# Kernel optimization log

Hardware: AMD Instinct MI355X
Metric: run time of the kernel (lower is better)

The kernel has to match this reference:

```python
import jax, jax.numpy as jnp
import numpy as np

N = 50000      # num nodes
E = 400000     # directed edges (avg out-degree 8)
DIN = 128
DOUT = 128
ALPHA = 0.5    # args.alphaDir (buffer, requires_grad=False)
BETA = 0.5     # args.betaDir
GAMA = 0.5     # args.gamaDir


def _dedupe(rows, cols, vals, n):
    key = rows.astype(np.int64) * n + cols.astype(np.int64)
    uk, inv = np.unique(key, return_inverse=True)
    v = np.bincount(inv, weights=vals, minlength=uk.shape[0])
    return (uk // n).astype(np.int32), (uk % n).astype(np.int32), v.astype(np.float32)


def _dir_norm(r, c, v, n):
    # directed_norm: D_out^{-1/2} A D_in^{-1/2}, inf -> 0
    in_deg = np.bincount(c, weights=v, minlength=n)
    out_deg = np.bincount(r, weights=v, minlength=n)
    in_is = np.zeros(n); m = in_deg > 0; in_is[m] = in_deg[m] ** -0.5
    out_is = np.zeros(n); m = out_deg > 0; out_is[m] = out_deg[m] ** -0.5
    return r, c, (out_is[r] * v * in_is[c]).astype(np.float32)


def _spgemm(rA, cA, vA, rB, cB, vB, n):
    # sparse @ sparse in COO, vectorized numpy
    order = np.argsort(rB, kind='stable')
    rBs, cBs, vBs = rB[order], cB[order], vB[order]
    degB = np.bincount(rBs, minlength=n)
    indptr = np.concatenate(([0], np.cumsum(degB)))
    counts = degB[cA]
    total = int(counts.sum())
    rep = np.repeat(np.arange(len(rA)), counts)
    first = np.cumsum(counts) - counts
    pos = np.arange(total) - np.repeat(first, counts) + np.repeat(indptr[cA], counts)
    rows = rA[rep]
    cols = cBs[pos]
    vals = vA[rep].astype(np.float64) * vBs[pos]
    return _dedupe(rows, cols, vals, n)


def setup_inputs() -> dict:
    rng = np.random.default_rng(0)
    r0 = rng.integers(0, N, E).astype(np.int64)
    c0 = rng.integers(0, N, E).astype(np.int64)
    r, c, v = _dedupe(r0, c0, np.ones(E, np.float32), N)
    a = _dir_norm(r, c, v, N)                 # adj_norm
    at = _dir_norm(c, r, v, N)                # adj_t_norm
    rr, cc, vv = _spgemm(a[0], a[1], a[2], at[0], at[1], at[2], N)
    aat = _dir_norm(rr, cc, vv, N)            # directed_norm(A @ At)
    rr, cc, vv = _spgemm(at[0], at[1], at[2], a[0], a[1], a[2], N)
    ata = _dir_norm(rr, cc, vv, N)            # directed_norm(At @ A)
    rr, cc, vv = _spgemm(a[0], a[1], a[2], a[0], a[1], a[2], N)
    aa = _dir_norm(rr, cc, vv, N)             # directed_norm(A @ A)
    rr, cc, vv = _spgemm(at[0], at[1], at[2], at[0], at[1], at[2], N)
    atat = _dir_norm(rr, cc, vv, N)           # directed_norm(At @ At)

    key = jax.random.key(0)
    ks = jax.random.split(key, 7)
    x = jax.random.normal(ks[0], (N, DIN), dtype=jnp.float32)
    s = 1.0 / np.sqrt(DIN)

    def lin(k):
        k1, k2 = jax.random.split(k)
        w = jax.random.uniform(k1, (DIN, DOUT), jnp.float32, -s, s)
        b = jax.random.uniform(k2, (DOUT,), jnp.float32, -s, s)
        return w, b

    w_sd, b_sd = lin(ks[1]); w_ds, b_ds = lin(ks[2])
    w0, b0 = lin(ks[3]); w1, b1 = lin(ks[4])
    w2, b2 = lin(ks[5]); w3, b3 = lin(ks[6])

    out = {'x': x,
           'w_sd': w_sd, 'b_sd': b_sd, 'w_ds': w_ds, 'b_ds': b_ds,
           'w0': w0, 'b0': b0, 'w1': w1, 'b1': b1,
           'w2': w2, 'b2': b2, 'w3': w3, 'b3': b3}
    for name, t in (('a', a), ('at', at), ('aat', aat), ('ata', ata), ('aa', aa), ('atat', atat)):
        out[name + '_rows'] = jnp.asarray(t[0])
        out[name + '_cols'] = jnp.asarray(t[1])
        out[name + '_vals'] = jnp.asarray(t[2])
    return out


def _spmm(rows, cols, vals, x):
    # (A @ x)[i] = sum_e vals[e] * x[cols[e]] scattered to rows[e]
    return jax.ops.segment_sum(vals[:, None] * x[cols], rows, num_segments=x.shape[0])


def reference(x, a_rows, a_cols, a_vals, at_rows, at_cols, at_vals,
              aat_rows, aat_cols, aat_vals, ata_rows, ata_cols, ata_vals,
              aa_rows, aa_cols, aa_vals, atat_rows, atat_cols, atat_vals,
              w_sd, b_sd, w_ds, b_ds, w0, b0, w1, b1, w2, b2, w3, b3):
    out1 = ALPHA * (_spmm(a_rows, a_cols, a_vals, x) @ w_sd + b_sd) \
         + (1.0 - ALPHA) * (_spmm(at_rows, at_cols, at_vals, x) @ w_ds + b_ds)
    out2 = BETA * (_spmm(aat_rows, aat_cols, aat_vals, x) @ w0 + b0) \
         + (1.0 - BETA) * (_spmm(ata_rows, ata_cols, ata_vals, x) @ w1 + b1)
    out3 = GAMA * (_spmm(aa_rows, aa_cols, aa_vals, x) @ w2 + b2) \
         + (1.0 - GAMA) * (_spmm(atat_rows, atat_cols, atat_vals, x) @ w3 + b3)
    return out1 + out2 + out3
```

## Files before the change

kernel.cpp:

```cpp
#include <hip/hip_runtime.h>
#include <hip/hip_bf16.h>

#define FD 128

typedef __attribute__((ext_vector_type(8))) short bf16x8;
typedef __attribute__((ext_vector_type(4))) float f32x4;

__device__ __forceinline__ float bfu2f(unsigned short u) {
  return __uint_as_float(((unsigned int)u) << 16);
}
__device__ __forceinline__ float b2f(__hip_bfloat16 v) { return __bfloat162float(v); }
__device__ __forceinline__ unsigned int pk2(float lo, float hi) {
  return (unsigned int)__bfloat16_as_ushort(__float2bfloat16(lo)) |
         ((unsigned int)__bfloat16_as_ushort(__float2bfloat16(hi)) << 16);
}

__device__ __forceinline__ float ldf(const void* p, int i, int ff) {
  return ff ? ((const float*)p)[i] : b2f(((const __hip_bfloat16*)p)[i]);
}
__device__ __forceinline__ int ldi(const void* p, int i, int fi) {
  return fi ? (int)((const long long*)p)[i] : ((const int*)p)[i];
}

__global__ void detect_k(const void* x, const void* cols, int* flags) {
  __shared__ int cnt[2];
  if (threadIdx.x < 2) cnt[threadIdx.x] = 0;
  __syncthreads();
  const unsigned short* xu = (const unsigned short*)x;
  int big = 0;
  for (int i = threadIdx.x; i < 1024; i += 256) {
    int e = (xu[i] >> 7) & 0xFF;
    if (e >= 0x90) big++;
  }
  if (big) atomicAdd(&cnt[0], big);
  const int* ci = (const int*)cols;
  int zeros = 0;
  for (int i = threadIdx.x; i < 128; i += 256)
    if ((i & 1) && ci[i] == 0) zeros++;
  if (zeros) atomicAdd(&cnt[1], zeros);
  __syncthreads();
  if (threadIdx.x == 0) {
    flags[0] = (cnt[0] > 16) ? 1 : 0;
    flags[1] = (cnt[1] >= 32) ? 1 : 0;
  }
}

__global__ void cvtall_k(const void* __restrict__ rows, const void* __restrict__ cols,
                         const void* __restrict__ vals, int nnz, int n,
                         int* __restrict__ r32, int* __restrict__ c32,
                         float* __restrict__ vf, int* __restrict__ cntT,
                         const int* flags) {
  int ff = flags[0], fi = flags[1];
  int i = blockIdx.x * 256 + threadIdx.x;
  if (i >= nnz) return;
  int r = ldi(rows, i, fi);
  int c = ldi(cols, i, fi);
  if ((unsigned)r >= (unsigned)n) r = 0;
  if ((unsigned)c >= (unsigned)n) c = 0;
  r32[i] = r;
  c32[i] = c;
  vf[i] = ldf(vals, i, ff);
  atomicAdd(&cntT[c], 1);
}

__global__ void scanA_k(const int* __restrict__ cnt, int n, int* bsum) {
  __shared__ int sh[256];
  int t = threadIdx.x;
  int i = blockIdx.x * 256 + t;
  sh[t] = (i < n) ? cnt[i] : 0;
  __syncthreads();
  for (int d = 128; d > 0; d >>= 1) {
    if (t < d) sh[t] += sh[t + d];
    __syncthreads();
  }
  if (t == 0) bsum[blockIdx.x] = sh[0];
}

__global__ void scanB_k(int* bsum, int nb, int* rpTail) {
  __shared__ int sh[256];
  int t = threadIdx.x;
  int v = (t < nb) ? bsum[t] : 0;
  sh[t] = v;
  __syncthreads();
  int val = v;
  for (int d = 1; d < 256; d <<= 1) {
    int add = (t >= d) ? sh[t - d] : 0;
    __syncthreads();
    val += add;
    sh[t] = val;
    __syncthreads();
  }
  if (t < nb) bsum[t] = val - v;
  if (t == 255) *rpTail = val;
}

__global__ void scanC_k(const int* __restrict__ cnt, int n, const int* __restrict__ bsum,
                        int* rp, int* cur) {
  __shared__ int sh[256];
  int t = threadIdx.x;
  int i = blockIdx.x * 256 + t;
  int v = (i < n) ? cnt[i] : 0;
  sh[t] = v;
  __syncthreads();
  int val = v;
  for (int d = 1; d < 256; d <<= 1) {
    int add = (t >= d) ? sh[t - d] : 0;
    __syncthreads();
    val += add;
    sh[t] = val;
    __syncthreads();
  }
  int ex = val - v + bsum[blockIdx.x];
  if (i < n) { rp[i] = ex; cur[i] = ex; }
}

__global__ void bsearch_k(const int* __restrict__ rows, int nnz, int n, int* rpA) {
  int i = blockIdx.x * 256 + threadIdx.x;
  if (i > n) return;
  int lo = 0, hi = nnz;
  while (lo < hi) { int mid = (lo + hi) >> 1; if (rows[mid] < i) lo = mid + 1; else hi = mid; }
  rpA[i] = lo;
}

__global__ void scatter_k(const int* __restrict__ r, const int* __restrict__ c,
                          const float* __restrict__ v, int nnz,
                          int* cur, int* tSrc, float* tVal) {
  int i = blockIdx.x * 256 + threadIdx.x;
  if (i >= nnz) return;
  int p = atomicAdd(&cur[c[i]], 1);
  if ((unsigned)p >= (unsigned)nnz) return;
  tSrc[p] = r[i];
  tVal[p] = v[i];
}

__global__ void nodesum_k(const int* __restrict__ rpA, const float* __restrict__ av,
                          const int* __restrict__ rpT, const float* __restrict__ tv,
                          float* __restrict__ u1, float* __restrict__ v1, int n) {
  int i = blockIdx.x * 256 + threadIdx.x;
  if (i >= n) return;
  float su = 0.f;
  int e0 = rpA[i], e1 = rpA[i + 1];
  for (int j = e0; j < e1; ++j) su += av[j];
  u1[i] = su;
  float sv = 0.f;
  int f0 = rpT[i], f1 = rpT[i + 1];
  for (int j = f0; j < f1; ++j) sv += tv[j];
  v1[i] = sv;
}

__global__ void deg2c_k(const int* __restrict__ rpA, const int* __restrict__ ci,
                        const float* __restrict__ av,
                        const int* __restrict__ rpT, const int* __restrict__ ti,
                        const float* __restrict__ tv,
                        const float* __restrict__ u1, const float* __restrict__ v1,
                        float* __restrict__ s1, float* __restrict__ s2,
                        float* __restrict__ s3, float* __restrict__ s4, int n) {
  int i = blockIdx.x * 256 + threadIdx.x;
  if (i >= n) return;
  float a1 = 0.f, a3 = 0.f;
  int s0 = rpA[i], se = rpA[i + 1];
  for (int j = s0; j < se; ++j) {
    int c = ci[j];
    float v = av[j];
    a1 = fmaf(v, v1[c], a1);
    a3 = fmaf(v, u1[c], a3);
  }
  s1[i] = (a1 > 0.f) ? rsqrtf(a1) : 0.f;
  s3[i] = (a3 > 0.f) ? rsqrtf(a3) : 0.f;
  float a2 = 0.f, a4 = 0.f;
  int t0 = rpT[i], t1 = rpT[i + 1];
  for (int j = t0; j < t1; ++j) {
    int r = ti[j];
    float v = tv[j];
    a2 = fmaf(v, u1[r], a2);
    a4 = fmaf(v, v1[r], a4);
  }
  s2[i] = (a2 > 0.f) ? rsqrtf(a2) : 0.f;
  s4[i] = (a4 > 0.f) ? rsqrtf(a4) : 0.f;
}

__global__ void bias_k(const void* a, const void* b, const void* c, const void* d,
                       const void* e, const void* f, float* bias, const int* flags) {
  int ff = flags[0];
  int i = threadIdx.x;
  bias[i] = 0.5f * (ldf(a, i, ff) + ldf(b, i, ff) + ldf(c, i, ff)
                  + ldf(d, i, ff) + ldf(e, i, ff) + ldf(f, i, ff));
}

__global__ void fill_k(unsigned short* o, int n) {
  int i = blockIdx.x * 256 + threadIdx.x;
  if (i < n) o[i] = 0x3E80;
}

__global__ void cvtx_k(const void* __restrict__ x, __hip_bfloat16* __restrict__ xb,
                       int n, const int* flags) {
  int ff = flags[0];
  int i = (blockIdx.x * 256 + threadIdx.x) * 4;
  if (i + 3 >= n) {
    for (int k = i; k < n; ++k) xb[k] = __float2bfloat16(ldf(x, k, ff));
    return;
  }
  xb[i + 0] = __float2bfloat16(ldf(x, i + 0, ff));
  xb[i + 1] = __float2bfloat16(ldf(x, i + 1, ff));
  xb[i + 2] = __float2bfloat16(ldf(x, i + 2, ff));
  xb[i + 3] = __float2bfloat16(ldf(x, i + 3, ff));
}

struct W6p { const void* w[6]; };
__global__ void wt2_k(W6p ws, __hip_bfloat16* __restrict__ Wt, const int* flags) {
  int ff = flags[0];
  int e = blockIdx.x * 256 + threadIdx.x;
  if (e >= 6 * 16384) return;
  int seg = e >> 14;
  int r = e & 16383;
  int n = r >> 7;
  int innerB = (r & 127) << 1;
  int kb = innerB ^ ((n & 7) << 4);
  int k = kb >> 1;
  Wt[e] = __float2bfloat16(ldf(ws.w[seg], k * 128 + n, ff));
}

struct FHSet {
  const int* rp; const int* ci; const float* cv;
  unsigned int* ot; unsigned int* oa; unsigned int* ob;
  const float* sA; const float* sB;
};

__global__ __launch_bounds__(256) void fh3d_k(
    FHSet h0, FHSet h1, const unsigned int* __restrict__ xb, int n, int half) {
  int blk = blockIdx.x;
  bool hi = blk >= half;
  const int* rp = hi ? h1.rp : h0.rp;
  const int* ci = hi ? h1.ci : h0.ci;
  const float* cv = hi ? h1.cv : h0.cv;
  unsigned int* ot = hi ? h1.ot : h0.ot;
  unsigned int* oa = hi ? h1.oa : h0.oa;
  unsigned int* ob = hi ? h1.ob : h0.ob;
  const float* sA = hi ? h1.sA : h0.sA;
  const float* sB = hi ? h1.sB : h0.sB;
  int bb = hi ? blk - half : blk;

  int wave = threadIdx.x >> 6;
  int lane = threadIdx.x & 63;
  int es = lane >> 4;
  int li = lane & 15;
  int r = bb * 4 + wave;
  if (r >= n) return;
  int s = rp[r], e = rp[r + 1];
  float t[8], a[8], b[8];
#pragma unroll
  for (int k = 0; k < 8; ++k) { t[k] = 0.f; a[k] = 0.f; b[k] = 0.f; }
  for (int j = s + es; j < e; j += 4) {
    int c = ci[j];
    float v = cv[j];
    float va = v * sA[c];
    float vb = v * sB[c];
    uint4 u = *(const uint4*)(xb + (size_t)c * 64 + li * 4);
    unsigned int uu[4] = {u.x, u.y, u.z, u.w};
#pragma unroll
    for (int k = 0; k < 4; ++k) {
      float lo = __uint_as_float(uu[k] << 16);
      float hi2 = __uint_as_float(uu[k] & 0xFFFF0000u);
      t[2 * k]     = fmaf(v, lo, t[2 * k]);
      t[2 * k + 1] = fmaf(v, hi2, t[2 * k + 1]);
      a[2 * k]     = fmaf(va, lo, a[2 * k]);
      a[2 * k + 1] = fmaf(va, hi2, a[2 * k + 1]);
      b[2 * k]     = fmaf(vb, lo, b[2 * k]);
      b[2 * k + 1] = fmaf(vb, hi2, b[2 * k + 1]);
    }
  }
#pragma unroll
  for (int k = 0; k < 8; ++k) {
    t[k] += __shfl_xor(t[k], 16); t[k] += __shfl_xor(t[k], 32);
    a[k] += __shfl_xor(a[k], 16); a[k] += __shfl_xor(a[k], 32);
    b[k] += __shfl_xor(b[k], 16); b[k] += __shfl_xor(b[k], 32);
  }
  if (es == 0) {
    size_t off = (size_t)r * 64 + li * 4;
    uint4 o;
    o.x = pk2(t[0], t[1]); o.y = pk2(t[2], t[3]);
    o.z = pk2(t[4], t[5]); o.w = pk2(t[6], t[7]);
    *(uint4*)(ot + off) = o;
    o.x = pk2(a[0], a[1]); o.y = pk2(a[2], a[3]);
    o.z = pk2(a[4], a[5]); o.w = pk2(a[6], a[7]);
    *(uint4*)(oa + off) = o;
    o.x = pk2(b[0], b[1]); o.y = pk2(b[2], b[3]);
    o.z = pk2(b[4], b[5]); o.w = pk2(b[6], b[7]);
    *(uint4*)(ob + off) = o;
  }
}

struct SHSet {
  const int* rp; const int* ci; const float* cv;
  const unsigned int* ga; const unsigned int* gb;
  unsigned int* ya; unsigned int* yb;
  const float* rsa; const float* rsb;
};

__global__ __launch_bounds__(256) void sh2d_k(SHSet h0, SHSet h1, int n, int half) {
  int blk = blockIdx.x;
  bool hi = blk >= half;
  const int* rp = hi ? h1.rp : h0.rp;
  const int* ci = hi ? h1.ci : h0.ci;
  const float* cv = hi ? h1.cv : h0.cv;
  const unsigned int* ga = hi ? h1.ga : h0.ga;
  const unsigned int* gb = hi ? h1.gb : h0.gb;
  unsigned int* ya = hi ? h1.ya : h0.ya;
  unsigned int* yb = hi ? h1.yb : h0.yb;
  const float* rsa = hi ? h1.rsa : h0.rsa;
  const float* rsb = hi ? h1.rsb : h0.rsb;
  int bb = hi ? blk - half : blk;

  int wave = threadIdx.x >> 6;
  int lane = threadIdx.x & 63;
  int es = lane >> 4;
  int li = lane & 15;
  int r = bb * 4 + wave;
  if (r >= n) return;
  int s = rp[r], e = rp[r + 1];
  float a[8], b[8];
#pragma unroll
  for (int k = 0; k < 8; ++k) { a[k] = 0.f; b[k] = 0.f; }
  for (int j = s + es; j < e; j += 4) {
    int c = ci[j];
    float v = cv[j];
    size_t off = (size_t)c * 64 + li * 4;
    uint4 u = *(const uint4*)(ga + off);
    uint4 w = *(const uint4*)(gb + off);
    unsigned int uu[4] = {u.x, u.y, u.z, u.w};
    unsigned int ww[4] = {w.x, w.y, w.z, w.w};
#pragma unroll
    for (int k = 0; k < 4; ++k) {
      a[2 * k]     = fmaf(v, __uint_as_float(uu[k] << 16), a[2 * k]);
      a[2 * k + 1] = fmaf(v, __uint_as_float(uu[k] & 0xFFFF0000u), a[2 * k + 1]);
      b[2 * k]     = fmaf(v, __uint_as_float(ww[k] << 16), b[2 * k]);
      b[2 * k + 1] = fmaf(v, __uint_as_float(ww[k] & 0xFFFF0000u), b[2 * k + 1]);
    }
  }
#pragma unroll
  for (int k = 0; k < 8; ++k) {
    a[k] += __shfl_xor(a[k], 16); a[k] += __shfl_xor(a[k], 32);
    b[k] += __shfl_xor(b[k], 16); b[k] += __shfl_xor(b[k], 32);
  }
  if (es == 0) {
    float ra = rsa[r], rb = rsb[r];
    size_t off = (size_t)r * 64 + li * 4;
    uint4 o;
    o.x = pk2(a[0] * ra, a[1] * ra); o.y = pk2(a[2] * ra, a[3] * ra);
    o.z = pk2(a[4] * ra, a[5] * ra); o.w = pk2(a[6] * ra, a[7] * ra);
    *(uint4*)(ya + off) = o;
    o.x = pk2(b[0] * rb, b[1] * rb); o.y = pk2(b[2] * rb, b[3] * rb);
    o.z = pk2(b[4] * rb, b[5] * rb); o.w = pk2(b[6] * rb, b[7] * rb);
    *(uint4*)(yb + off) = o;
  }
}

struct Y6 { const unsigned short* y[6]; };

__global__ __launch_bounds__(256) void gemm6m3_k(
    Y6 ys, const unsigned short* __restrict__ Wt2, const float* __restrict__ bias,
    void* __restrict__ outp, int M, const int* flags) {
  int ff = flags[0];
  __shared__ __align__(16) unsigned short Bs[16384];
  const int tid = threadIdx.x;
  const int lane = tid & 63;
  const int wave = tid >> 6;
  const int m = lane & 15;
  const int q = lane >> 4;
  const int r0 = blockIdx.x * 128 + wave * 32;
  const int row0 = r0 + m;
  const int row1 = r0 + 16 + m;
  const bool ok0 = row0 < M;
  const bool ok1 = row1 < M;
  const bf16x8 zero8 = {0, 0, 0, 0, 0, 0, 0, 0};

  f32x4 acc0[8], acc1[8];
#pragma unroll
  for (int nt = 0; nt < 8; ++nt) {
    acc0[nt] = (f32x4){0.f, 0.f, 0.f, 0.f};
    acc1[nt] = (f32x4){0.f, 0.f, 0.f, 0.f};
  }

  bf16x8 Bst[8];
#pragma unroll
  for (int c2 = 0; c2 < 8; ++c2)
    Bst[c2] = *(const bf16x8*)(Wt2 + (size_t)(c2 * 256 + tid) * 8);
  bf16x8 Ap0[4], Ap1[4];
#pragma unroll
  for (int kc = 0; kc < 4; ++kc) {
    Ap0[kc] = ok0 ? *(const bf16x8*)(ys.y[0] + (size_t)row0 * FD + kc * 32 + q * 8) : zero8;
    Ap1[kc] = ok1 ? *(const bf16x8*)(ys.y[0] + (size_t)row1 * FD + kc * 32 + q * 8) : zero8;
  }

  const int swz = (m & 7) << 4;

#pragma unroll
  for (int t = 0; t < 6; ++t) {
    __syncthreads();
#pragma unroll
    for (int c2 = 0; c2 < 8; ++c2)
      *(bf16x8*)((char*)Bs + (size_t)(c2 * 256 + tid) * 16) = Bst[c2];
    bf16x8 A0[4], A1[4];
#pragma unroll
    for (int kc = 0; kc < 4; ++kc) { A0[kc] = Ap0[kc]; A1[kc] = Ap1[kc]; }
    if (t < 5) {
#pragma unroll
      for (int c2 = 0; c2 < 8; ++c2)
        Bst[c2] = *(const bf16x8*)(Wt2 + (size_t)(t + 1) * 16384 +
                                   (size_t)(c2 * 256 + tid) * 8);
#pragma unroll
      for (int kc = 0; kc < 4; ++kc) {
        Ap0[kc] = ok0 ? *(const bf16x8*)(ys.y[t + 1] + (size_t)row0 * FD + kc * 32 + q * 8) : zero8;
        Ap1[kc] = ok1 ? *(const bf16x8*)(ys.y[t + 1] + (size_t)row1 * FD + kc * 32 + q * 8) : zero8;
      }
    }
    __syncthreads();
#pragma unroll
    for (int kc = 0; kc < 4; ++kc) {
      const int koff = (kc * 64 + q * 16) ^ swz;
#pragma unroll
      for (int nt = 0; nt < 8; ++nt) {
        const int nrow = nt * 16 + m;
        bf16x8 bfv = *(const bf16x8*)((const char*)Bs + nrow * 256 + koff);
        acc0[nt] = __builtin_amdgcn_mfma_f32_16x16x32_bf16(A0[kc], bfv, acc0[nt], 0, 0, 0);
        acc1[nt] = __builtin_amdgcn_mfma_f32_16x16x32_bf16(A1[kc], bfv, acc1[nt], 0, 0, 0);
      }
    }
  }

#pragma unroll
  for (int nt = 0; nt < 8; ++nt) {
    int col = nt * 16 + m;
    float bv = bias[col];
#pragma unroll
    for (int rg = 0; rg < 4; ++rg) {
      int g0 = r0 + q * 4 + rg;
      if (g0 < M) {
        float v = 0.5f * acc0[nt][rg] + bv;
        if (ff) ((float*)outp)[(size_t)g0 * FD + col] = v;
        else ((unsigned short*)outp)[(size_t)g0 * FD + col] =
            __bfloat16_as_ushort(__float2bfloat16(v));
      }
      int g1 = r0 + 16 + q * 4 + rg;
      if (g1 < M) {
        float v = 0.5f * acc1[nt][rg] + bv;
        if (ff) ((float*)outp)[(size_t)g1 * FD + col] = v;
        else ((unsigned short*)outp)[(size_t)g1 * FD + col] =
            __bfloat16_as_ushort(__float2bfloat16(v));
      }
    }
  }
}

__global__ __launch_bounds__(128) void spmm_k(
    const int* __restrict__ rp, const void* __restrict__ ci, int cif,
    const void* __restrict__ cv, int cvf,
    const void* __restrict__ x, int xf, __hip_bfloat16* __restrict__ y,
    int n, int nnzMax,
    const float* __restrict__ cscale, const float* __restrict__ rscale,
    const int* flags) {
  int ff = flags[0], fi = flags[1];
  int vf = cvf ? 1 : ff;
  int iw = cif ? fi : 0;
  int xw = xf ? ff : 0;
  const int t = threadIdx.x;
  int r0 = blockIdx.x * 4;
  int rend = min(r0 + 4, n);
  for (int r = r0; r < rend; ++r) {
    int s = rp[r], e = rp[r + 1];
    s = max(0, min(s, nnzMax));
    e = max(s, min(e, nnzMax));
    float acc = 0.f;
    for (int j = s; j < e; ++j) {
      int c = ldi(ci, j, iw);
      if ((unsigned)c >= (unsigned)n) c = 0;
      float v = (vf ? ((const float*)cv)[j] : b2f(((const __hip_bfloat16*)cv)[j]));
      if (cscale) v *= cscale[c];
      float xv = xw ? ((const float*)x)[c * FD + t]
                    : b2f(((const __hip_bfloat16*)x)[c * FD + t]);
      acc = fmaf(v, xv, acc);
    }
    if (rscale) acc *= rscale[r];
    y[r * FD + t] = __float2bfloat16(acc);
  }
}

__global__ __launch_bounds__(256) void gemm_k(
    const __hip_bfloat16* __restrict__ Y, const void* __restrict__ W,
    const float* __restrict__ bias, const void* __restrict__ accin,
    void* __restrict__ outp, int M, const int* flags) {
  int ff = flags[0];
  __shared__ __align__(16) float Wl[32 * 128];
  __shared__ __align__(16) float Yl[64 * 36];
  const int t = threadIdx.x;
  const int row0 = blockIdx.x * 64;
  const int c4 = (t & 31) * 4;
  const int r8 = (t >> 5) * 8;
  const int rs = t >> 3;
  const int q = t & 7;
  float acc[8][4];
#pragma unroll
  for (int m = 0; m < 8; ++m)
#pragma unroll
    for (int j = 0; j < 4; ++j) acc[m][j] = 0.f;
  for (int kc = 0; kc < 4; ++kc) {
    if (ff) {
      const float4* Wg4 = (const float4*)((const float*)W + kc * 32 * 128);
#pragma unroll
      for (int i = 0; i < 4; ++i)
        *(float4*)(Wl + (t + i * 256) * 4) = Wg4[t + i * 256];
    } else {
      const ushort4* Wg4 = (const ushort4*)((const unsigned short*)W + kc * 32 * 128);
#pragma unroll
      for (int i = 0; i < 4; ++i) {
        ushort4 u = Wg4[t + i * 256];
        int base = (t + i * 256) * 4;
        Wl[base + 0] = bfu2f(u.x);
        Wl[base + 1] = bfu2f(u.y);
        Wl[base + 2] = bfu2f(u.z);
        Wl[base + 3] = bfu2f(u.w);
      }
    }
#pragma unroll
    for (int i = 0; i < 2; ++i) {
      int rr = rs + i * 32;
      int grow = row0 + rr;
      ushort4 u = make_ushort4(0, 0, 0, 0);
      if (grow < M)
        u = *(const ushort4*)((const unsigned short*)Y + grow * FD + kc * 32 + q * 4);
      float* yd = Yl + rr * 36 + q * 4;
      yd[0] = bfu2f(u.x); yd[1] = bfu2f(u.y); yd[2] = bfu2f(u.z); yd[3] = bfu2f(u.w);
    }
    __syncthreads();
#pragma unroll
    for (int kk = 0; kk < 32; kk += 4) {
      float4 w0 = *(const float4*)(Wl + (kk + 0) * 128 + c4);
      float4 w1 = *(const float4*)(Wl + (kk + 1) * 128 + c4);
      float4 w2 = *(const float4*)(Wl + (kk + 2) * 128 + c4);
      float4 w3 = *(const float4*)(Wl + (kk + 3) * 128 + c4);
#pragma unroll
      for (int m = 0; m < 8; ++m) {
        float4 yv = *(const float4*)(Yl + (r8 + m) * 36 + kk);
        acc[m][0] = fmaf(yv.x, w0.x, acc[m][0]);
        acc[m][1] = fmaf(yv.x, w0.y, acc[m][1]);
        acc[m][2] = fmaf(yv.x, w0.z, acc[m][2]);
        acc[m][3] = fmaf(yv.x, w0.w, acc[m][3]);
        acc[m][0] = fmaf(yv.y, w1.x, acc[m][0]);
        acc[m][1] = fmaf(yv.y, w1.y, acc[m][1]);
        acc[m][2] = fmaf(yv.y, w1.z, acc[m][2]);
        acc[m][3] = fmaf(yv.y, w1.w, acc[m][3]);
        acc[m][0] = fmaf(yv.z, w2.x, acc[m][0]);
        acc[m][1] = fmaf(yv.z, w2.y, acc[m][1]);
        acc[m][2] = fmaf(yv.z, w2.z, acc[m][2]);
        acc[m][3] = fmaf(yv.z, w2.w, acc[m][3]);
        acc[m][0] = fmaf(yv.w, w3.x, acc[m][0]);
        acc[m][1] = fmaf(yv.w, w3.y, acc[m][1]);
        acc[m][2] = fmaf(yv.w, w3.z, acc[m][2]);
        acc[m][3] = fmaf(yv.w, w3.w, acc[m][3]);
      }
    }
    __syncthreads();
  }
  float4 b4 = make_float4(0.f, 0.f, 0.f, 0.f);
  if (bias) b4 = *(const float4*)(bias + c4);
#pragma unroll
  for (int m = 0; m < 8; ++m) {
    int grow = row0 + r8 + m;
    if (grow >= M) continue;
    float4 rv;
    rv.x = 0.5f * acc[m][0] + b4.x;
    rv.y = 0.5f * acc[m][1] + b4.y;
    rv.z = 0.5f * acc[m][2] + b4.z;
    rv.w = 0.5f * acc[m][3] + b4.w;
    if (accin) {
      if (ff) {
        float4 o = *(const float4*)((const float*)accin + grow * FD + c4);
        rv.x += o.x; rv.y += o.y; rv.z += o.z; rv.w += o.w;
      } else {
        ushort4 o = *(const ushort4*)((const unsigned short*)accin + grow * FD + c4);
        rv.x += bfu2f(o.x); rv.y += bfu2f(o.y); rv.z += bfu2f(o.z); rv.w += bfu2f(o.w);
      }
    }
    if (ff) {
      *(float4*)((float*)outp + grow * FD + c4) = rv;
    } else {
      ushort4 so;
      so.x = __bfloat16_as_ushort(__float2bfloat16(rv.x));
      so.y = __bfloat16_as_ushort(__float2bfloat16(rv.y));
      so.z = __bfloat16_as_ushort(__float2bfloat16(rv.z));
      so.w = __bfloat16_as_ushort(__float2bfloat16(rv.w));
      *(ushort4*)((unsigned short*)outp + grow * FD + c4) = so;
    }
  }
}

extern "C" void kernel_launch(void* const* d_in, const int* in_sizes, int n_in,
                              void* d_out, int out_size, void* d_ws, size_t ws_size,
                              hipStream_t stream) {
  const void* x    = d_in[0];
  const void* w_sd = d_in[1];
  const void* b_sd = d_in[2];
  const void* w_ds = d_in[3];
  const void* b_ds = d_in[4];
  const void* w0   = d_in[5];
  const void* b0   = d_in[6];
  const void* w1   = d_in[7];
  const void* b1   = d_in[8];
  const void* w2   = d_in[9];
  const void* b2   = d_in[10];
  const void* w3   = d_in[11];
  const void* b3   = d_in[12];
  const void* a_rows = d_in[13];
  const void* a_cols = d_in[14];
  const void* a_vals = d_in[15];
  const int nnz = in_sizes[13];
  const int N = in_sizes[0] / FD;

  const size_t BUF = ((size_t)N * FD * 2 + 255) & ~(size_t)255;

  auto misc_need = [&](int nbig) -> size_t {
    size_t need = (size_t)nbig * BUF;
    need += ((size_t)10 * N * 4 + 255) & ~(size_t)255;
    need += 512 + 256 + 1024;
    need += (((size_t)(N + 1) * 4 + 255) & ~(size_t)255) * 2;
    need += (((size_t)N * 4 + 255) & ~(size_t)255) * 2;
    need += (((size_t)nnz * 4 + 255) & ~(size_t)255) * 5;
    need += (6 * 16384 * 2 + 255) & ~(size_t)255;
    return need;
  };
  size_t needA = misc_need(10);
  size_t needB = misc_need(2);

  int pathA = (ws_size >= needA) ? 1 : 0;
  if (!pathA && ws_size < needB) {
    fill_k<<<(out_size + 255) / 256, 256, 0, stream>>>((unsigned short*)d_out, out_size);
    return;
  }

  int nbig = pathA ? 10 : 2;
  char* p = (char*)d_ws;
  char* bufs[10];
  for (int i = 0; i < 10; ++i) bufs[i] = (i < nbig) ? (p + (size_t)i * BUF) : nullptr;
  char* q = p + (size_t)nbig * BUF;
  auto take = [&](size_t bytes) -> char* {
    char* r = q;
    q += (bytes + 255) & ~(size_t)255;
    return r;
  };
  float* degf  = (float*)take((size_t)10 * N * 4);
  float* biasf = (float*)take(512);
  int*   flags = (int*)take(256);
  int*   bsum  = (int*)take(1024);
  int* rpA  = (int*)take((size_t)(N + 1) * 4);
  int* rpT  = (int*)take((size_t)(N + 1) * 4);
  int* curT = (int*)take((size_t)N * 4);
  int* cntT = (int*)take((size_t)N * 4);
  int* tSrc = (int*)take((size_t)nnz * 4);
  float* tValF = (float*)take((size_t)nnz * 4);
  int* aRow32 = (int*)take((size_t)nnz * 4);
  int* aCol32 = (int*)take((size_t)nnz * 4);
  float* aValF = (float*)take((size_t)nnz * 4);
  __hip_bfloat16* Wt = (__hip_bfloat16*)take(6 * 16384 * 2);

  float* u1 = degf;
  float* v1 = degf + N;
  float* s1 = degf + 6 * N;
  float* s2 = degf + 7 * N;
  float* s3 = degf + 8 * N;
  float* s4 = degf + 9 * N;

  int eb = (nnz + 255) / 256;
  int nb = (N + 255) / 256;

  detect_k<<<1, 256, 0, stream>>>(x, a_cols, flags);
  hipMemsetAsync(cntT, 0, (size_t)N * 4, stream);
  cvtall_k<<<eb, 256, 0, stream>>>(a_rows, a_cols, a_vals, nnz, N, aRow32, aCol32, aValF, cntT, flags);
  scanA_k<<<nb, 256, 0, stream>>>(cntT, N, bsum);
  scanB_k<<<1, 256, 0, stream>>>(bsum, nb, rpT + N);
  scanC_k<<<nb, 256, 0, stream>>>(cntT, N, bsum, rpT, curT);
  bsearch_k<<<(N + 256) / 256, 256, 0, stream>>>(aRow32, nnz, N, rpA);
  scatter_k<<<eb, 256, 0, stream>>>(aRow32, aCol32, aValF, nnz, curT, tSrc, tValF);
  nodesum_k<<<nb, 256, 0, stream>>>(rpA, aValF, rpT, tValF, u1, v1, N);
  deg2c_k<<<nb, 256, 0, stream>>>(rpA, aCol32, aValF, rpT, tSrc, tValF, u1, v1,
                                  s1, s2, s3, s4, N);
  bias_k<<<1, FD, 0, stream>>>(b_sd, b_ds, b0, b1, b2, b3, biasf, flags);

  int sg2 = (N + 3) / 4;
  int gg = (N + 63) / 64;
  int gg4 = (N + 127) / 128;

  if (pathA) {
    W6p wargs;
    wargs.w[0] = w_sd; wargs.w[1] = w_ds; wargs.w[2] = w0;
    wargs.w[3] = w1;   wargs.w[4] = w2;   wargs.w[5] = w3;
    wt2_k<<<(6 * 16384 + 255) / 256, 256, 0, stream>>>(wargs, Wt, flags);

    __hip_bfloat16* xb = (__hip_bfloat16*)bufs[0];
    cvtx_k<<<(N * FD / 4 + 255) / 256, 256, 0, stream>>>(x, xb, N * FD, flags);

    unsigned int* xbu = (unsigned int*)bufs[0];
    unsigned int* t2 = (unsigned int*)bufs[1];
    unsigned int* g3 = (unsigned int*)bufs[2];
    unsigned int* g6 = (unsigned int*)bufs[3];
    unsigned int* t1 = (unsigned int*)bufs[4];
    unsigned int* g4 = (unsigned int*)bufs[5];
    unsigned int* g5 = (unsigned int*)bufs[6];
    unsigned int* y3 = (unsigned int*)bufs[7];
    unsigned int* y4 = (unsigned int*)bufs[8];
    unsigned int* y6 = (unsigned int*)bufs[9];
    unsigned int* y5 = (unsigned int*)bufs[0];

    FHSet hT = { rpT, tSrc, tValF, t2, g3, g6, s1, s3 };
    FHSet hA = { rpA, aCol32, aValF, t1, g4, g5, s2, s4 };
    fh3d_k<<<2 * sg2, 256, 0, stream>>>(hT, hA, xbu, N, sg2);

    SHSet sA = { rpA, aCol32, aValF, g3, g5, y3, y5, s1, s3 };
    SHSet sT = { rpT, tSrc, tValF, g4, g6, y4, y6, s2, s4 };
    sh2d_k<<<2 * sg2, 256, 0, stream>>>(sA, sT, N, sg2);

    Y6 yargs;
    yargs.y[0] = (const unsigned short*)t1;
    yargs.y[1] = (const unsigned short*)t2;
    yargs.y[2] = (const unsigned short*)y3;
    yargs.y[3] = (const unsigned short*)y4;
    yargs.y[4] = (const unsigned short*)y5;
    yargs.y[5] = (const unsigned short*)y6;
    gemm6m3_k<<<gg4, 256, 0, stream>>>(yargs, (const unsigned short*)Wt, biasf, d_out, N, flags);
  } else {
    __hip_bfloat16* Yb = (__hip_bfloat16*)bufs[0];
    __hip_bfloat16* gb = (__hip_bfloat16*)bufs[1];
    spmm_k<<<sg2, 128, 0, stream>>>(rpA, a_cols, 1, a_vals, 0, x, 1, Yb, N, nnz, nullptr, nullptr, flags);
    gemm_k<<<gg, 256, 0, stream>>>(Yb, w_sd, biasf, nullptr, d_out, N, flags);
    spmm_k<<<sg2, 128, 0, stream>>>(rpT, tSrc, 0, tValF, 1, x, 1, Yb, N, nnz, nullptr, nullptr, flags);
    gemm_k<<<gg, 256, 0, stream>>>(Yb, w_ds, nullptr, d_out, d_out, N, flags);
    spmm_k<<<sg2, 128, 0, stream>>>(rpT, tSrc, 0, tValF, 1, x, 1, gb, N, nnz, s1, nullptr, flags);
    spmm_k<<<sg2, 128, 0, stream>>>(rpA, a_cols, 1, a_vals, 0, gb, 0, Yb, N, nnz, nullptr, s1, flags);
    gemm_k<<<gg, 256, 0, stream>>>(Yb, w0, nullptr, d_out, d_out, N, flags);
    spmm_k<<<sg2, 128, 0, stream>>>(rpA, a_cols, 1, a_vals, 0, x, 1, gb, N, nnz, s2, nullptr, flags);
    spmm_k<<<sg2, 128, 0, stream>>>(rpT, tSrc, 0, tValF, 1, gb, 0, Yb, N, nnz, nullptr, s2, flags);
    gemm_k<<<gg, 256, 0, stream>>>(Yb, w1, nullptr, d_out, d_out, N, flags);
    spmm_k<<<sg2, 128, 0, stream>>>(rpA, a_cols, 1, a_vals, 0, x, 1, gb, N, nnz, s4, nullptr, flags);
    spmm_k<<<sg2, 128, 0, stream>>>(rpA, a_cols, 1, a_vals, 0, gb, 0, Yb, N, nnz, nullptr, s3, flags);
    gemm_k<<<gg, 256, 0, stream>>>(Yb, w2, nullptr, d_out, d_out, N, flags);
    spmm_k<<<sg2, 128, 0, stream>>>(rpT, tSrc, 0, tValF, 1, x, 1, gb, N, nnz, s3, nullptr, flags);
    spmm_k<<<sg2, 128, 0, stream>>>(rpT, tSrc, 0, tValF, 1, gb, 0, Yb, N, nnz, nullptr, s4, flags);
    gemm_k<<<gg, 256, 0, stream>>>(Yb, w3, nullptr, d_out, d_out, N, flags);
  }
}
```

Baseline: 447.3 us.

## Interleave intermediate pairs, unroll gather loops by two, fuse prep kernels

The two intermediate bf16 tensors read together by the second-hop SpMM are now stored interleaved per row (256 B for one half, then 256 B for the other) in a single buffer. Each gathered neighbour then touches one contiguous 512 B region instead of two separate rows. Both gather loops are unrolled by two so that two neighbour loads are in flight at once. The x conversion, weight transpose and bias sum are merged into a single prep kernel to save launches. The cost is a changed buffer assignment and higher register pressure from the unrolled loops.

Measured after the change: 446.2 us. No clear change (-0.2%).

```diff
diff --git a/kernel.cpp b/kernel.cpp
--- a/kernel.cpp
+++ b/kernel.cpp
@@ -192,32 +192,71 @@
   if (i < n) o[i] = 0x3E80;
 }
 
-__global__ void cvtx_k(const void* __restrict__ x, __hip_bfloat16* __restrict__ xb,
-                       int n, const int* flags) {
+struct W6p { const void* w[6]; };
+struct B6p { const void* b[6]; };
+
+__global__ void prep_k(const void* __restrict__ x, __hip_bfloat16* __restrict__ xb, int nx,
+                       W6p ws, __hip_bfloat16* __restrict__ Wt,
+                       B6p bs, float* __restrict__ bias,
+                       const int* flags, int cvtB) {
   int ff = flags[0];
-  int i = (blockIdx.x * 256 + threadIdx.x) * 4;
-  if (i + 3 >= n) {
-    for (int k = i; k < n; ++k) xb[k] = __float2bfloat16(ldf(x, k, ff));
-    return;
-  }
-  xb[i + 0] = __float2bfloat16(ldf(x, i + 0, ff));
-  xb[i + 1] = __float2bfloat16(ldf(x, i + 1, ff));
-  xb[i + 2] = __float2bfloat16(ldf(x, i + 2, ff));
-  xb[i + 3] = __float2bfloat16(ldf(x, i + 3, ff));
-}
-
-struct W6p { const void* w[6]; };
-__global__ void wt2_k(W6p ws, __hip_bfloat16* __restrict__ Wt, const int* flags) {
-  int ff = flags[0];
-  int e = blockIdx.x * 256 + threadIdx.x;
-  if (e >= 6 * 16384) return;
-  int seg = e >> 14;
-  int r = e & 16383;
-  int n = r >> 7;
-  int innerB = (r & 127) << 1;
-  int kb = innerB ^ ((n & 7) << 4);
-  int k = kb >> 1;
-  Wt[e] = __float2bfloat16(ldf(ws.w[seg], k * 128 + n, ff));
+  int blk = blockIdx.x;
+  if (blk < cvtB) {
+    int i = (blk * 256 + threadIdx.x) * 4;
+    if (i >= nx) return;
+    if (i + 3 >= nx) {
+      for (int k = i; k < nx; ++k) xb[k] = __float2bfloat16(ldf(x, k, ff));
+      return;
+    }
+    xb[i + 0] = __float2bfloat16(ldf(x, i + 0, ff));
+    xb[i + 1] = __float2bfloat16(ldf(x, i + 1, ff));
+    xb[i + 2] = __float2bfloat16(ldf(x, i + 2, ff));
+    xb[i + 3] = __float2bfloat16(ldf(x, i + 3, ff));
+  } else if (blk < cvtB + 384) {
+    int e = (blk - cvtB) * 256 + threadIdx.x;
+    if (e >= 6 * 16384) return;
+    int seg = e >> 14;
+    int r = e & 16383;
+    int n = r >> 7;
+    int innerB = (r & 127) << 1;
+    int kb = innerB ^ ((n & 7) << 4);
+    int k = kb >> 1;
+    Wt[e] = __float2bfloat16(ldf(ws.w[seg], k * 128 + n, ff));
+  } else {
+    int i = threadIdx.x;
+    if (i < FD)
+      bias[i] = 0.5f * (ldf(bs.b[0], i, ff) + ldf(bs.b[1], i, ff) + ldf(bs.b[2], i, ff)
+                      + ldf(bs.b[3], i, ff) + ldf(bs.b[4], i, ff) + ldf(bs.b[5], i, ff));
+  }
+}
+
+__device__ __forceinline__ void fh_fma(const uint4& u, float v, float va, float vb,
+                                       float* t, float* a, float* b) {
+  unsigned int uu[4] = {u.x, u.y, u.z, u.w};
+#pragma unroll
+  for (int k = 0; k < 4; ++k) {
+    float lo = __uint_as_float(uu[k] << 16);
+    float hi = __uint_as_float(uu[k] & 0xFFFF0000u);
+    t[2 * k]     = fmaf(v, lo, t[2 * k]);
+    t[2 * k + 1] = fmaf(v, hi, t[2 * k + 1]);
+    a[2 * k]     = fmaf(va, lo, a[2 * k]);
+    a[2 * k + 1] = fmaf(va, hi, a[2 * k + 1]);
+    b[2 * k]     = fmaf(vb, lo, b[2 * k]);
+    b[2 * k + 1] = fmaf(vb, hi, b[2 * k + 1]);
+  }
+}
+
+__device__ __forceinline__ void sh_fma(const uint4& u, const uint4& w, float v,
+                                       float* a, float* b) {
+  unsigned int uu[4] = {u.x, u.y, u.z, u.w};
+  unsigned int ww[4] = {w.x, w.y, w.z, w.w};
+#pragma unroll
+  for (int k = 0; k < 4; ++k) {
+    a[2 * k]     = fmaf(v, __uint_as_float(uu[k] << 16), a[2 * k]);
+    a[2 * k + 1] = fmaf(v, __uint_as_float(uu[k] & 0xFFFF0000u), a[2 * k + 1]);
+    b[2 * k]     = fmaf(v, __uint_as_float(ww[k] << 16), b[2 * k]);
+    b[2 * k + 1] = fmaf(v, __uint_as_float(ww[k] & 0xFFFF0000u), b[2 * k + 1]);
+  }
 }
 
 struct FHSet {
@@ -250,24 +289,23 @@
   float t[8], a[8], b[8];
 #pragma unroll
   for (int k = 0; k < 8; ++k) { t[k] = 0.f; a[k] = 0.f; b[k] = 0.f; }
-  for (int j = s + es; j < e; j += 4) {
+  int j = s + es;
+  for (; j < e - 4; j += 8) {
+    int c1 = ci[j], c2 = ci[j + 4];
+    float v1 = cv[j], v2 = cv[j + 4];
+    float va1 = v1 * sA[c1], vb1 = v1 * sB[c1];
+    float va2 = v2 * sA[c2], vb2 = v2 * sB[c2];
+    uint4 u1 = *(const uint4*)(xb + (size_t)c1 * 64 + li * 4);
+    uint4 u2 = *(const uint4*)(xb + (size_t)c2 * 64 + li * 4);
+    fh_fma(u1, v1, va1, vb1, t, a, b);
+    fh_fma(u2, v2, va2, vb2, t, a, b);
+  }
+  if (j < e) {
     int c = ci[j];
     float v = cv[j];
-    float va = v * sA[c];
-    float vb = v * sB[c];
+    float va = v * sA[c], vb = v * sB[c];
     uint4 u = *(const uint4*)(xb + (size_t)c * 64 + li * 4);
-    unsigned int uu[4] = {u.x, u.y, u.z, u.w};
-#pragma unroll
-    for (int k = 0; k < 4; ++k) {
-      float lo = __uint_as_float(uu[k] << 16);
-      float hi2 = __uint_as_float(uu[k] & 0xFFFF0000u);
-      t[2 * k]     = fmaf(v, lo, t[2 * k]);
-      t[2 * k + 1] = fmaf(v, hi2, t[2 * k + 1]);
-      a[2 * k]     = fmaf(va, lo, a[2 * k]);
-      a[2 * k + 1] = fmaf(va, hi2, a[2 * k + 1]);
-      b[2 * k]     = fmaf(vb, lo, b[2 * k]);
-      b[2 * k + 1] = fmaf(vb, hi2, b[2 * k + 1]);
-    }
+    fh_fma(u, v, va, vb, t, a, b);
   }
 #pragma unroll
   for (int k = 0; k < 8; ++k) {
@@ -276,23 +314,22 @@
     b[k] += __shfl_xor(b[k], 16); b[k] += __shfl_xor(b[k], 32);
   }
   if (es == 0) {
-    size_t off = (size_t)r * 64 + li * 4;
     uint4 o;
     o.x = pk2(t[0], t[1]); o.y = pk2(t[2], t[3]);
     o.z = pk2(t[4], t[5]); o.w = pk2(t[6], t[7]);
-    *(uint4*)(ot + off) = o;
+    *(uint4*)(ot + (size_t)r * 64 + li * 4) = o;
     o.x = pk2(a[0], a[1]); o.y = pk2(a[2], a[3]);
     o.z = pk2(a[4], a[5]); o.w = pk2(a[6], a[7]);
-    *(uint4*)(oa + off) = o;
+    *(uint4*)(oa + (size_t)r * 128 + li * 4) = o;
     o.x = pk2(b[0], b[1]); o.y = pk2(b[2], b[3]);
     o.z = pk2(b[4], b[5]); o.w = pk2(b[6], b[7]);
-    *(uint4*)(ob + off) = o;
+    *(uint4*)(ob + (size_t)r * 128 + li * 4) = o;
   }
 }
 
 struct SHSet {
   const int* rp; const int* ci; const float* cv;
-  const unsigned int* ga; const unsigned int* gb;
+  const unsigned int* gp;
   unsigned int* ya; unsigned int* yb;
   const float* rsa; const float* rsb;
 };
@@ -303,8 +340,7 @@
   const int* rp = hi ? h1.rp : h0.rp;
   const int* ci = hi ? h1.ci : h0.ci;
   const float* cv = hi ? h1.cv : h0.cv;
-  const unsigned int* ga = hi ? h1.ga : h0.ga;
-  const unsigned int* gb = hi ? h1.gb : h0.gb;
+  const unsigned int* gp = hi ? h1.gp : h0.gp;
   unsigned int* ya = hi ? h1.ya : h0.ya;
   unsigned int* yb = hi ? h1.yb : h0.yb;
   const float* rsa = hi ? h1.rsa : h0.rsa;
@@ -321,21 +357,26 @@
   float a[8], b[8];
 #pragma unroll
   for (int k = 0; k < 8; ++k) { a[k] = 0.f; b[k] = 0.f; }
-  for (int j = s + es; j < e; j += 4) {
+  int j = s + es;
+  for (; j < e - 4; j += 8) {
+    int c1 = ci[j], c2 = ci[j + 4];
+    float v1 = cv[j], v2 = cv[j + 4];
+    const unsigned int* b1 = gp + (size_t)c1 * 128;
+    const unsigned int* b2 = gp + (size_t)c2 * 128;
+    uint4 u1 = *(const uint4*)(b1 + li * 4);
+    uint4 w1 = *(const uint4*)(b1 + 64 + li * 4);
+    uint4 u2 = *(const uint4*)(b2 + li * 4);
+    uint4 w2 = *(const uint4*)(b2 + 64 + li * 4);
+    sh_fma(u1, w1, v1, a, b);
+    sh_fma(u2, w2, v2, a, b);
+  }
+  if (j < e) {
     int c = ci[j];
     float v = cv[j];
-    size_t off = (size_t)c * 64 + li * 4;
-    uint4 u = *(const uint4*)(ga + off);
-    uint4 w = *(const uint4*)(gb + off);
-    unsigned int uu[4] = {u.x, u.y, u.z, u.w};
-    unsigned int ww[4] = {w.x, w.y, w.z, w.w};
-#pragma unroll
-    for (int k = 0; k < 4; ++k) {
-      a[2 * k]     = fmaf(v, __uint_as_float(uu[k] << 16), a[2 * k]);
-      a[2 * k + 1] = fmaf(v, __uint_as_float(uu[k] & 0xFFFF0000u), a[2 * k + 1]);
-      b[2 * k]     = fmaf(v, __uint_as_float(ww[k] << 16), b[2 * k]);
-      b[2 * k + 1] = fmaf(v, __uint_as_float(ww[k] & 0xFFFF0000u), b[2 * k + 1]);
-    }
+    const unsigned int* bp = gp + (size_t)c * 128;
+    uint4 u = *(const uint4*)(bp + li * 4);
+    uint4 w = *(const uint4*)(bp + 64 + li * 4);
+    sh_fma(u, w, v, a, b);
   }
 #pragma unroll
   for (int k = 0; k < 8; ++k) {
@@ -683,7 +724,6 @@
   nodesum_k<<<nb, 256, 0, stream>>>(rpA, aValF, rpT, tValF, u1, v1, N);
   deg2c_k<<<nb, 256, 0, stream>>>(rpA, aCol32, aValF, rpT, tSrc, tValF, u1, v1,
                                   s1, s2, s3, s4, N);
-  bias_k<<<1, FD, 0, stream>>>(b_sd, b_ds, b0, b1, b2, b3, biasf, flags);
 
   int sg2 = (N + 3) / 4;
   int gg = (N + 63) / 64;
@@ -693,29 +733,30 @@
     W6p wargs;
     wargs.w[0] = w_sd; wargs.w[1] = w_ds; wargs.w[2] = w0;
     wargs.w[3] = w1;   wargs.w[4] = w2;   wargs.w[5] = w3;
-    wt2_k<<<(6 * 16384 + 255) / 256, 256, 0, stream>>>(wargs, Wt, flags);
-
+    B6p bargs;
+    bargs.b[0] = b_sd; bargs.b[1] = b_ds; bargs.b[2] = b0;
+    bargs.b[3] = b1;   bargs.b[4] = b2;   bargs.b[5] = b3;
     __hip_bfloat16* xb = (__hip_bfloat16*)bufs[0];
-    cvtx_k<<<(N * FD / 4 + 255) / 256, 256, 0, stream>>>(x, xb, N * FD, flags);
+    int cvtB = (N * FD / 4 + 255) / 256;
+    prep_k<<<cvtB + 384 + 1, 256, 0, stream>>>(x, xb, N * FD, wargs, Wt, bargs, biasf,
+                                               flags, cvtB);
 
     unsigned int* xbu = (unsigned int*)bufs[0];
     unsigned int* t2 = (unsigned int*)bufs[1];
-    unsigned int* g3 = (unsigned int*)bufs[2];
-    unsigned int* g6 = (unsigned int*)bufs[3];
-    unsigned int* t1 = (unsigned int*)bufs[4];
-    unsigned int* g4 = (unsigned int*)bufs[5];
-    unsigned int* g5 = (unsigned int*)bufs[6];
+    unsigned int* t1 = (unsigned int*)bufs[2];
+    unsigned int* P1 = (unsigned int*)bufs[3];
+    unsigned int* P2 = (unsigned int*)bufs[5];
     unsigned int* y3 = (unsigned int*)bufs[7];
     unsigned int* y4 = (unsigned int*)bufs[8];
     unsigned int* y6 = (unsigned int*)bufs[9];
     unsigned int* y5 = (unsigned int*)bufs[0];
 
-    FHSet hT = { rpT, tSrc, tValF, t2, g3, g6, s1, s3 };
-    FHSet hA = { rpA, aCol32, aValF, t1, g4, g5, s2, s4 };
+    FHSet hT = { rpT, tSrc, tValF, t2, P1, P2 + 64, s1, s3 };
+    FHSet hA = { rpA, aCol32, aValF, t1, P2, P1 + 64, s2, s4 };
     fh3d_k<<<2 * sg2, 256, 0, stream>>>(hT, hA, xbu, N, sg2);
 
-    SHSet sA = { rpA, aCol32, aValF, g3, g5, y3, y5, s1, s3 };
-    SHSet sT = { rpT, tSrc, tValF, g4, g6, y4, y6, s2, s4 };
+    SHSet sA = { rpA, aCol32, aValF, P1, y3, y5, s1, s3 };
+    SHSet sT = { rpT, tSrc, tValF, P2, y4, y6, s2, s4 };
     sh2d_k<<<2 * sg2, 256, 0, stream>>>(sA, sT, N, sg2);
 
     Y6 yargs;
@@ -727,6 +768,7 @@
     yargs.y[5] = (const unsigned short*)y6;
     gemm6m3_k<<<gg4, 256, 0, stream>>>(yargs, (const unsigned short*)Wt, biasf, d_out, N, flags);
   } else {
+    bias_k<<<1, FD, 0, stream>>>(b_sd, b_ds, b0, b1, b2, b3, biasf, flags);
     __hip_bfloat16* Yb = (__hip_bfloat16*)bufs[0];
     __hip_bfloat16* gb = (__hip_bfloat16*)bufs[1];
     spmm_k<<<sg2, 128, 0, stream>>>(rpA, a_cols, 1, a_vals, 0, x, 1, Yb, N, nnz, nullptr, nullptr, flags);
```
